# Kernel optimization log

Hardware: AMD Instinct MI355X
Metric: run time of the kernel (lower is better)

The kernel has to match this reference:

```python
import jax, jax.numpy as jnp
import numpy as np
from jax.scipy.stats import norm

B, IN, H0, H1, OUT = 1024, 2048, 4096, 4096, 1000
EPS_CDF = 1e-5
DECAY = 0.01
NEG_SLOPE = 0.01  # LeakyReLU default slope


def setup_inputs() -> dict:
    key = jax.random.key(0)
    ks = iter(jax.random.split(key, 40))
    rn = lambda shp, s=1.0: s * jax.random.normal(next(ks), shp, dtype=jnp.float32)
    inp = {}
    inp['x'] = rn((B, IN))
    inp['z_w'] = rn((IN,), 0.02)
    for nm, (o, i) in zip(['0', '1', 'o'], [(H0, IN), (H1, H0), (OUT, H1)]):
        inp['w_mu' + nm] = rn((o, i), 0.02)
        inp['w_ls' + nm] = rn((o, i), 0.1) - 2.0  # log-sigma ~ -2 => sigma ~ 0.13
        inp['b_mu' + nm] = rn((o,), 0.02)
        inp['b_ls' + nm] = rn((o,), 0.1) - 2.0
        inp['eps_w' + nm] = rn((o, i))
        inp['eps_b' + nm] = rn((o,))
    inp['pfz0'] = jax.random.uniform(next(ks), (B, H0), dtype=jnp.float32)
    inp['pfz1'] = jax.random.uniform(next(ks), (B, H1), dtype=jnp.float32)
    inp['y'] = jax.random.randint(next(ks), (B,), 0, OUT, dtype=jnp.int32)
    inp['mz0'] = jax.random.randint(next(ks), (B, H0), 0, 2, dtype=jnp.int32)
    inp['mz1'] = jax.random.randint(next(ks), (B, H1), 0, 2, dtype=jnp.int32)
    inp['mask_mu0'] = jax.random.randint(next(ks), (H0,), 0, 2, dtype=jnp.int32)
    inp['mask_mu1'] = jax.random.randint(next(ks), (H1,), 0, 2, dtype=jnp.int32)
    inp['data_set_size'] = 60000
    return inp


def _bayes_layer(h, w_mu, w_ls, b_mu, b_ls, eps_w, eps_b, mz, mask_mu, pfz):
    sw = jnp.exp(w_ls)
    sb = jnp.exp(b_ls)
    w = w_mu + sw * eps_w          # reparameterized weight sample
    b = b_mu + sb * eps_b
    h = h @ w.T + b                # F.linear
    h = jnp.where(h >= 0, h, NEG_SLOPE * h)  # LeakyReLU
    mzf = mz.astype(h.dtype)
    m = mzf * mask_mu.astype(h.dtype)[None, :]   # [B, h]
    mult = m.shape[1] / (m.sum(1) + 1e-6)        # rescale multiplier per sample
    h = h * m * mult[:, None]
    # GFN forward-flow log-prob of the z-mask
    p = jnp.clip(pfz, 1e-6, 1.0 - 1e-6)
    flow = (mzf * jnp.log(p) + (1.0 - mzf) * jnp.log(1.0 - p)).sum()
    # Gaussian CDF likelihood of sampled weights/biases (finite-difference density)
    pw = norm.cdf(w + EPS_CDF, w_mu, sw) - norm.cdf(w - EPS_CDF, w_mu, sw)
    pb = norm.cdf(b + EPS_CDF, b_mu, sb) - norm.cdf(b - EPS_CDF, b_mu, sb)
    flow = flow + jnp.log(pw).sum() + jnp.log(pb).sum()
    return h, flow


def reference(x, z_w, w_mu0, w_ls0, b_mu0, b_ls0, eps_w0, eps_b0,
              w_mu1, w_ls1, b_mu1, b_ls1, eps_w1, eps_b1,
              w_muo, w_lso, b_muo, b_lso, eps_wo, eps_bo,
              pfz0, pfz1, y, mz0, mz1, mask_mu0, mask_mu1, data_set_size):
    loss = (x @ z_w).sum()  # total flow estimator Z
    h, f0 = _bayes_layer(x, w_mu0, w_ls0, b_mu0, b_ls0, eps_w0, eps_b0, mz0, mask_mu0, pfz0)
    loss = loss + f0
    h, f1 = _bayes_layer(h, w_mu1, w_ls1, b_mu1, b_ls1, eps_w1, eps_b1, mz1, mask_mu1, pfz1)
    loss = loss + f1
    # output BayesLinear (sampled)
    wo = w_muo + jnp.exp(w_lso) * eps_wo
    bo = b_muo + jnp.exp(b_lso) * eps_bo
    pred = h @ wo.T + bo  # [B, OUT]
    logp = jax.nn.log_softmax(pred, axis=-1)
    ce = -jnp.take_along_axis(logp, y[:, None].astype(jnp.int32), axis=1).mean()
    loss = loss + jnp.float32(data_set_size) * ce  # NLL
    wd = DECAY * ((w_mu0 ** 2).sum() + jnp.exp(w_ls0).sum()
                  + (w_mu1 ** 2).sum() + jnp.exp(w_ls1).sum())
    loss = (loss + wd) ** 2
    return pred, loss
```

## Files before the change

kernel.cpp:

```cpp
#include <hip/hip_runtime.h>
#include <math.h>

#define B_SZ 1024
#define IN_SZ 2048
#define H0_SZ 4096
#define H1_SZ 4096
#define OUT_SZ 1000

typedef _Float16 f16;
typedef __attribute__((ext_vector_type(4))) _Float16 f16x4;
typedef __attribute__((ext_vector_type(8))) _Float16 f16x8;
typedef __attribute__((ext_vector_type(4))) float f32x4;

#define OFF_N0     0ULL
#define OFF_N1     4ULL
#define OFF_MSUM0  256ULL
#define OFF_MSUM1  4352ULL
#define OFF_CPOS0  8448ULL
#define OFF_CPOS1  24832ULL
#define OFF_IDX0   41216ULL
#define OFF_IDX1   57600ULL
#define OFF_PXZ    73984ULL
#define OFF_PFL    82176ULL
#define OFF_PCE    98560ULL
#define OFF_PB     106752ULL
#define OFF_PW     107776ULL
#define OFF_BS0    370688ULL
#define OFF_BS1    387072ULL
#define OFF_BSO    403456ULL
#define OFF_XH     407552ULL
#define OFF_XL     4601856ULL
#define OFF_H0H    8796160ULL
#define OFF_H0L    17184768ULL
#define OFF_H1H    25573376ULL
#define OFF_H1L    33961984ULL
#define OFF_W0CH   42350592ULL
#define OFF_W0CL   59127808ULL
#define OFF_W1CH   75905024ULL
#define OFF_W1CL   109459456ULL
#define OFF_WOCH   143013888ULL
#define OFF_WOCL   151402496ULL
#define OFF_PART   159791104ULL

#define PSTRIDE_H  2560
#define PSTRIDE_O  1024

#define PA_W0   1024
#define PA_FL0  1280
#define PA_SX   1536
#define PA_B0   1552
#define L0_G    640
#define L0_W1   1664
#define L0_FL1  1920
#define L0_B1   1936
#define L1_G    640
#define L1_WO   890
#define L1_BO   894

__device__ __forceinline__ void gload_lds16(const void* g, void* l)
{
    __builtin_amdgcn_global_load_lds((const __attribute__((address_space(1))) void*)g,
                                     (__attribute__((address_space(3))) void*)l, 16, 0, 0);
}

__device__ __forceinline__ void reduce4_store(double v0, double v1, double v2, double v3,
                                              double* dst)
{
    __shared__ double sh[4][4];
    double v[4] = {v0, v1, v2, v3};
    int lane = threadIdx.x & 63, wid = threadIdx.x >> 6;
#pragma unroll
    for (int a = 0; a < 4; ++a) {
        double x = v[a];
#pragma unroll
        for (int o = 32; o > 0; o >>= 1) x += __shfl_down(x, o, 64);
        if (lane == 0) sh[a][wid] = x;
    }
    __syncthreads();
    if (threadIdx.x == 0) {
        dst[0] = sh[0][0] + sh[0][1] + sh[0][2] + sh[0][3];
        dst[1] = sh[1][0] + sh[1][1] + sh[1][2] + sh[1][3];
        dst[2] = sh[2][0] + sh[2][1] + sh[2][2] + sh[2][3];
        dst[3] = sh[3][0] + sh[3][1] + sh[3][2] + sh[3][3];
    }
}

__device__ __forceinline__ void reduce1_store(double v, double* dst)
{
    __shared__ double sh1[4];
    int lane = threadIdx.x & 63, wid = threadIdx.x >> 6;
#pragma unroll
    for (int o = 32; o > 0; o >>= 1) v += __shfl_down(v, o, 64);
    if (lane == 0) sh1[wid] = v;
    __syncthreads();
    if (threadIdx.x == 0) dst[0] = sh1[0] + sh1[1] + sh1[2] + sh1[3];
}

__global__ __launch_bounds__(1024) void idxbuild_kernel(
    const int* __restrict__ mask0, const int* __restrict__ mask1,
    int* __restrict__ cpos0, int* __restrict__ idx0, int* __restrict__ n0,
    int* __restrict__ cpos1, int* __restrict__ idx1, int* __restrict__ n1)
{
    __shared__ int sh[1024];
    const int t = threadIdx.x;
    const int pass = blockIdx.x;
    const int* mask = pass ? mask1 : mask0;
    int* cpos = pass ? cpos1 : cpos0;
    int* idx = pass ? idx1 : idx0;
    int* np = pass ? n1 : n0;
    int4 m = ((const int4*)mask)[t];
    int s = m.x + m.y + m.z + m.w;
    sh[t] = s;
    __syncthreads();
    for (int o = 1; o < 1024; o <<= 1) {
        int v = (t >= o) ? sh[t - o] : 0;
        __syncthreads();
        sh[t] += v;
        __syncthreads();
    }
    int run = sh[t] - s;
    int4 cp;
    cp.x = run; cp.y = run + m.x; cp.z = cp.y + m.y; cp.w = cp.z + m.z;
    ((int4*)cpos)[t] = cp;
    if (m.x) idx[cp.x] = 4 * t + 0;
    if (m.y) idx[cp.y] = 4 * t + 1;
    if (m.z) idx[cp.z] = 4 * t + 2;
    if (m.w) idx[cp.w] = 4 * t + 3;
    if (t == 1023) *np = sh[1023];
}


__device__ void role_splitx(int rb, const float4* x, const float4* zw,
                            f16x4* xh, f16x4* xl, double* pxz)
{
    const int n4 = B_SZ * IN_SZ / 4;
    double s = 0;
    int i = rb * 256 + threadIdx.x;
    const int stride = 256 * 256;
    for (; i < n4; i += stride) {
        float4 v = x[i];
        float4 z = zw[i & (IN_SZ / 4 - 1)];
        s += (double)((v.x * z.x + v.y * z.y) + (v.z * z.z + v.w * z.w));
        f16 h0 = (f16)v.x, h1 = (f16)v.y, h2 = (f16)v.z, h3 = (f16)v.w;
        f16x4 hv = {h0, h1, h2, h3};
        f16x4 lv = {(f16)(v.x - (float)h0), (f16)(v.y - (float)h1),
                    (f16)(v.z - (float)h2), (f16)(v.w - (float)h3)};
        xh[i] = hv; xl[i] = lv;
    }
    reduce1_store(s, pxz + rb);
}

__device__ void role_flow4(int bb, const int* mz, const float* pfz, const int* maskmu,
                           float* msum, double* pfl)
{
    const int w = threadIdx.x >> 6, lane = threadIdx.x & 63;
    const int r = bb * 4 + w;
    const int4* m4 = (const int4*)(mz + (size_t)r * 4096);
    const float4* p4 = (const float4*)(pfz + (size_t)r * 4096);
    const int4* k4 = (const int4*)maskmu;
    int s = 0;
    double fl = 0;
    for (int i = lane; i < 1024; i += 64) {
        int4 m = m4[i];
        float4 p = p4[i];
        int4 k = k4[i];
        s += m.x * k.x + m.y * k.y + m.z * k.z + m.w * k.w;
        float a0 = fminf(fmaxf(p.x, 1e-6f), 1.0f - 1e-6f);
        float a1 = fminf(fmaxf(p.y, 1e-6f), 1.0f - 1e-6f);
        float a2 = fminf(fmaxf(p.z, 1e-6f), 1.0f - 1e-6f);
        float a3 = fminf(fmaxf(p.w, 1e-6f), 1.0f - 1e-6f);
        float g0 = logf(m.x ? a0 : 1.0f - a0);
        float g1 = logf(m.y ? a1 : 1.0f - a1);
        float g2 = logf(m.z ? a2 : 1.0f - a2);
        float g3 = logf(m.w ? a3 : 1.0f - a3);
        fl += (double)((g0 + g1) + (g2 + g3));
    }
#pragma unroll
    for (int o = 32; o > 0; o >>= 1) s += __shfl_down(s, o, 64);
    if (lane == 0) msum[r] = (float)s;
    reduce1_store(fl, pfl + bb);
}

template <int RED>
__device__ void role_bsample(int rb, const float* bmu, const float* bls, const float* beps,
                             float* out, int n, double* pb)
{
    int i = rb * 256 + threadIdx.x;
    float l = 0.f, e = 0.f;
    if (i < n) {
        l = bls[i]; e = beps[i];
        out[i] = fmaf(__expf(l), e, bmu[i]);
    }
    if (RED) {
        double sls = (i < n) ? (double)l : 0.0;
        double se2 = (i < n) ? (double)e * e : 0.0;
        reduce4_store(sls, se2, 0.0, 0.0, pb + (size_t)rb * 4);
    }
}

__device__ void role_w04(int bb, const float* mu, const float* ls, const float* eps,
                         const int* maskR, const int* cposR, f16* hi, double* pw)
{
    double sls = 0, se2 = 0, smu2 = 0, sex = 0;
#pragma unroll
    for (int rr = 0; rr < 4; ++rr) {
        const int r = bb * 4 + rr;
        const size_t rbb = (size_t)r * IN_SZ;
        const float4* m4 = (const float4*)(mu + rbb);
        const float4* l4 = (const float4*)(ls + rbb);
        const float4* e4 = (const float4*)(eps + rbb);
        const bool wr_ = maskR[r] != 0;
        const int drow = cposR[r];
        f16* hrow = hi + (size_t)drow * IN_SZ;
        for (int i = threadIdx.x; i < IN_SZ / 4; i += 256) {
            float4 m = m4[i], l = l4[i], e = e4[i];
            float g0 = __expf(l.x), g1 = __expf(l.y), g2 = __expf(l.z), g3 = __expf(l.w);
            float w0 = fmaf(g0, e.x, m.x), w1 = fmaf(g1, e.y, m.y);
            float w2 = fmaf(g2, e.z, m.z), w3 = fmaf(g3, e.w, m.w);
            sls += (double)((l.x + l.y) + (l.z + l.w));
            se2 += (double)((e.x * e.x + e.y * e.y) + (e.z * e.z + e.w * e.w));
            smu2 += (double)((m.x * m.x + m.y * m.y) + (m.z * m.z + m.w * m.w));
            sex += (double)((g0 + g1) + (g2 + g3));
            if (wr_) {
                f16x4 hv = {(f16)w0, (f16)w1, (f16)w2, (f16)w3};
                *(f16x4*)(hrow + i * 4) = hv;
            }
        }
    }
    reduce4_store(sls, se2, smu2, sex, pw + (size_t)bb * 4);
}

template <int ROWC, int RED>
__device__ void role_colc4(int bb, const float* mu, const float* ls, const float* eps,
                           const int* maskR, const int* cposR,
                           const int* maskC, const int* cposC, const int* pNc,
                           f16* hi, double* pw, f16* ldsH)
{
    const int t = threadIdx.x;
    const f16x8 z8 = {0, 0, 0, 0, 0, 0, 0, 0};
    for (int i = t; i < 512; i += 256) ((f16x8*)ldsH)[i] = z8;
    __syncthreads();
    double sls = 0, se2 = 0, smu2 = 0, sex = 0;
    const int n8 = ((*pNc + 127) >> 7) << 4;
#pragma unroll
    for (int rr = 0; rr < 4; ++rr) {
        const int r = bb * 4 + rr;
        const size_t rbb = (size_t)r * 4096;
        const float4* m4 = (const float4*)(mu + rbb);
        const float4* l4 = (const float4*)(ls + rbb);
        const float4* e4 = (const float4*)(eps + rbb);
        const bool wr_ = ROWC ? (maskR[r] != 0) : true;
        const int drow = ROWC ? cposR[r] : r;
        for (int i = t; i < 1024; i += 256) {
            float4 m = m4[i], l = l4[i], e = e4[i];
            float g0 = __expf(l.x), g1 = __expf(l.y), g2 = __expf(l.z), g3 = __expf(l.w);
            float w0 = fmaf(g0, e.x, m.x), w1 = fmaf(g1, e.y, m.y);
            float w2 = fmaf(g2, e.z, m.z), w3 = fmaf(g3, e.w, m.w);
            if (RED) {
                sls += (double)((l.x + l.y) + (l.z + l.w));
                se2 += (double)((e.x * e.x + e.y * e.y) + (e.z * e.z + e.w * e.w));
                smu2 += (double)((m.x * m.x + m.y * m.y) + (m.z * m.z + m.w * m.w));
                sex += (double)((g0 + g1) + (g2 + g3));
            }
            if (wr_) {
                int4 mc = ((const int4*)maskC)[i];
                int4 cp = ((const int4*)cposC)[i];
                if (mc.x) ldsH[cp.x] = (f16)w0;
                if (mc.y) ldsH[cp.y] = (f16)w1;
                if (mc.z) ldsH[cp.z] = (f16)w2;
                if (mc.w) ldsH[cp.w] = (f16)w3;
            }
        }
        __syncthreads();
        if (wr_) {
            f16x8* hd = (f16x8*)(hi + (size_t)drow * 4096);
            for (int i = t; i < n8; i += 256) hd[i] = ((const f16x8*)ldsH)[i];
        }
        __syncthreads();
    }
    if (RED) reduce4_store(sls, se2, smu2, sex, pw + (size_t)bb * 4);
}

template <int NSPLIT>
__device__ void gemm_body(int bid, f16* ldsbase,
                          const f16* Ah, const f16* Al, int SA,
                          const f16* Wh, int SW,
                          const int* pN, int NFIX, const int* pK, int KFIX,
                          float* P0, float* P1, float* P2, float* P3,
                          float* P4, float* P5, float* P6, float* P7, int pstride)
{
    const int c8 = bid & 7, j = bid >> 3;
    int nt, mt, z;
    if (NSPLIT == 4) {
        const int p = c8 + 8 * (j % 10);
        nt = p >> 2; z = p & 3; mt = j / 10;
    } else {
        const int p = c8 + 8 * (j & 7);
        nt = p >> 3; z = p & 7; mt = j >> 3;
    }
    const int nvalid = pN ? *pN : NFIX;
    const int bn = nt * 128;
    if (bn >= nvalid) return;
    const int bm = mt * 128;
    const int kvalid = pK ? *pK : KFIX;
    const int ktiles = (kvalid + 31) >> 5;
    const int prt = (ktiles + NSPLIT - 1) / NSPLIT;
    const int kt0 = z * prt;
    const int kt1 = min(ktiles, kt0 + prt);
    float* Cf = (z == 0) ? P0 : (z == 1) ? P1 : (z == 2) ? P2 : (z == 3) ? P3
              : (z == 4) ? P4 : (z == 5) ? P5 : (z == 6) ? P6 : P7;

    const int tid = threadIdx.x;
    const int wv = tid >> 6, lane = tid & 63;
    const int wr = wv >> 1, wc = wv & 1;
    const int l15 = lane & 15, l4 = lane >> 4;

    const f16* sg[6];
    int ldst[6];
#pragma unroll
    for (int i = 0; i < 6; ++i) {
        const int c = wv * 6 + i;
        const int plane = c >> 3, cidx = c & 7;
        const f16* base = (plane == 0) ? Ah : (plane == 1) ? Al : Wh;
        const int S_ = (plane < 2) ? SA : SW;
        const int rowb = (plane < 2) ? bm : bn;
        sg[i] = base + (size_t)(rowb + cidx * 16 + l15) * S_ + l4 * 8;
        ldst[i] = c * 512 + lane * 8;
    }

#define STAGE(KT, B) do { \
        _Pragma("unroll") \
        for (int i_ = 0; i_ < 6; ++i_) \
            gload_lds16(sg[i_] + (size_t)(KT) * 32, ldsbase + (B) * 12288 + ldst[i_]); \
    } while (0)

    f32x4 acc[4][4];
#pragma unroll
    for (int m = 0; m < 4; ++m)
#pragma unroll
        for (int n = 0; n < 4; ++n) acc[m][n] = (f32x4){0.f, 0.f, 0.f, 0.f};

    if (kt0 < kt1) {
        STAGE(kt0, 0);
        int cur = 0;
        for (int kt = kt0; kt < kt1; ++kt) {
            asm volatile("s_waitcnt vmcnt(0)" ::: "memory");
            __builtin_amdgcn_s_barrier();
            __builtin_amdgcn_sched_barrier(0);
            if (kt + 1 < kt1) STAGE(kt + 1, cur ^ 1);
            __builtin_amdgcn_sched_barrier(0);
            const f16* L = ldsbase + cur * 12288;
            f16x8 ah[4], al[4], wh[4];
#pragma unroll
            for (int m = 0; m < 4; ++m) {
                ah[m] = *(const f16x8*)(L + (wr * 4 + m) * 512 + lane * 8);
                al[m] = *(const f16x8*)(L + 4096 + (wr * 4 + m) * 512 + lane * 8);
            }
#pragma unroll
            for (int n = 0; n < 4; ++n)
                wh[n] = *(const f16x8*)(L + 8192 + (wc * 4 + n) * 512 + lane * 8);
            __builtin_amdgcn_s_setprio(1);
#pragma unroll
            for (int m = 0; m < 4; ++m)
#pragma unroll
                for (int n = 0; n < 4; ++n)
                    acc[m][n] = __builtin_amdgcn_mfma_f32_16x16x32_f16(ah[m], wh[n], acc[m][n], 0, 0, 0);
#pragma unroll
            for (int m = 0; m < 4; ++m)
#pragma unroll
                for (int n = 0; n < 4; ++n)
                    acc[m][n] = __builtin_amdgcn_mfma_f32_16x16x32_f16(al[m], wh[n], acc[m][n], 0, 0, 0);
            __builtin_amdgcn_s_setprio(0);
            cur ^= 1;
        }
    }
#undef STAGE

#pragma unroll
    for (int n = 0; n < 4; ++n) {
        const int c = bn + wc * 64 + n * 16 + l15;
        if (c >= pstride) continue;
#pragma unroll
        for (int m = 0; m < 4; ++m)
#pragma unroll
            for (int j2 = 0; j2 < 4; ++j2) {
                const int row = bm + wr * 64 + m * 16 + l4 * 4 + j2;
                Cf[(size_t)row * pstride + c] = acc[m][n][j2];
            }
    }
}

__global__ __launch_bounds__(256) void prepA_kernel(
    const float* __restrict__ x, const float* __restrict__ zw,
    const float* __restrict__ wmu0, const float* __restrict__ wls0, const float* __restrict__ weps0,
    const float* __restrict__ bmu0, const float* __restrict__ bls0, const float* __restrict__ beps0,
    const float* __restrict__ pfz0, const int* __restrict__ mz0,
    const int* __restrict__ mmu0, const int* __restrict__ cpos0,
    f16* __restrict__ xh, f16* __restrict__ xl, f16* __restrict__ w0ch,
    float* __restrict__ bs0, float* __restrict__ msum0,
    double* __restrict__ PXZ, double* __restrict__ PFL,
    double* __restrict__ PB, double* __restrict__ PW)
{
    const int b = blockIdx.x;
    if (b < PA_W0) {
        role_w04(b, wmu0, wls0, weps0, mmu0, cpos0, w0ch, PW);
    } else if (b < PA_FL0) {
        role_flow4(b - PA_W0, mz0, pfz0, mmu0, msum0, PFL);
    } else if (b < PA_SX) {
        role_splitx(b - PA_FL0, (const float4*)x, (const float4*)zw,
                    (f16x4*)xh, (f16x4*)xl, PXZ);
    } else {
        role_bsample<1>(b - PA_SX, bmu0, bls0, beps0, bs0, H0_SZ, PB);
    }
}

__global__ __launch_bounds__(256, 3) void gemmL0_kernel(
    const f16* __restrict__ xh, const f16* __restrict__ xl, const f16* __restrict__ w0ch,
    const int* __restrict__ n0p,
    float* __restrict__ A0, float* __restrict__ A1,
    float* __restrict__ A2, float* __restrict__ A3,
    const float* __restrict__ wmu1, const float* __restrict__ wls1, const float* __restrict__ weps1,
    const float* __restrict__ bmu1, const float* __restrict__ bls1, const float* __restrict__ beps1,
    const float* __restrict__ pfz1, const int* __restrict__ mz1,
    const int* __restrict__ mmu0, const int* __restrict__ mmu1,
    const int* __restrict__ cpos0, const int* __restrict__ cpos1,
    f16* __restrict__ w1ch, float* __restrict__ bs1, float* __restrict__ msum1,
    double* __restrict__ PFL, double* __restrict__ PB, double* __restrict__ PW)
{
    __shared__ __align__(16) f16 lds[2][12288];
    const int b = blockIdx.x;
    if (b < L0_G) {
        gemm_body<4>(b, &lds[0][0], xh, xl, IN_SZ, w0ch, IN_SZ, n0p, 0, nullptr, IN_SZ,
                     A0, A1, A2, A3, nullptr, nullptr, nullptr, nullptr, PSTRIDE_H);
    } else if (b < L0_W1) {
        role_colc4<1, 1>(b - L0_G, wmu1, wls1, weps1, mmu1, cpos1, mmu0, cpos0, n0p,
                         w1ch, PW + (size_t)4096 * 4, &lds[0][0]);
    } else if (b < L0_FL1) {
        role_flow4(b - L0_W1, mz1, pfz1, mmu1, msum1, PFL + 1024);
    } else {
        role_bsample<1>(b - L0_FL1, bmu1, bls1, beps1, bs1, H1_SZ, PB + 16 * 4);
    }
}

__global__ __launch_bounds__(256, 3) void gemmL1_kernel(
    const f16* __restrict__ h0h, const f16* __restrict__ h0l, const f16* __restrict__ w1ch,
    const int* __restrict__ n1p, const int* __restrict__ n0p,
    float* __restrict__ B0, float* __restrict__ B1,
    float* __restrict__ B2, float* __restrict__ B3,
    const float* __restrict__ wmuo, const float* __restrict__ wlso, const float* __restrict__ wepso,
    const float* __restrict__ bmuo, const float* __restrict__ blso, const float* __restrict__ bepso,
    const int* __restrict__ mmu1, const int* __restrict__ cpos1,
    f16* __restrict__ woch, float* __restrict__ bso)
{
    __shared__ __align__(16) f16 lds[2][12288];
    const int b = blockIdx.x;
    if (b < L1_G) {
        gemm_body<4>(b, &lds[0][0], h0h, h0l, 4096, w1ch, 4096, n1p, 0, n0p, 0,
                     B0, B1, B2, B3, nullptr, nullptr, nullptr, nullptr, PSTRIDE_H);
    } else if (b < L1_WO) {
        role_colc4<0, 0>(b - L1_G, wmuo, wlso, wepso, nullptr, nullptr, mmu1, cpos1, n1p,
                         woch, nullptr, &lds[0][0]);
    } else {
        role_bsample<0>(b - L1_WO, bmuo, blso, bepso, bso, OUT_SZ, nullptr);
    }
}

__global__ __launch_bounds__(256, 3) void gemmLo_kernel(
    const f16* __restrict__ h1h, const f16* __restrict__ h1l, const f16* __restrict__ woch,
    const int* __restrict__ n1p,
    float* __restrict__ Q0, float* __restrict__ Q1, float* __restrict__ Q2, float* __restrict__ Q3,
    float* __restrict__ Q4, float* __restrict__ Q5, float* __restrict__ Q6, float* __restrict__ Q7)
{
    __shared__ __align__(16) f16 lds[2][12288];
    gemm_body<8>(blockIdx.x, &lds[0][0], h1h, h1l, 4096, woch, 4096, nullptr, OUT_SZ, n1p, 0,
                 Q0, Q1, Q2, Q3, Q4, Q5, Q6, Q7, PSTRIDE_O);
}

__global__ __launch_bounds__(256) void combine4_kernel(
    const float* __restrict__ PA, const float* __restrict__ PB,
    const float* __restrict__ PC, const float* __restrict__ PD, int pstride,
    const float* __restrict__ bsamp, const int* __restrict__ idx,
    const int* __restrict__ mz, const float* __restrict__ msum,
    const int* __restrict__ pN,
    f16* __restrict__ Chh, f16* __restrict__ Chl)
{
    const int nv = *pN;
    const int bn = blockIdx.x * 64;
    const int bm = blockIdx.y * 64;
    const int t = threadIdx.x;
    const int c0 = bn + (t & 15) * 4;
    const int r0 = bm + (t >> 4);
#pragma unroll
    for (int rr = 0; rr < 4; ++rr) {
        const int row = r0 + rr * 16;
        const float mult = 4096.0f / (msum[row] + 1e-6f);
        float sv[4] = {0.f, 0.f, 0.f, 0.f};
        if (c0 < pstride) {
            float4 a = *(const float4*)(PA + (size_t)row * pstride + c0);
            float4 b = *(const float4*)(PB + (size_t)row * pstride + c0);
            float4 c = *(const float4*)(PC + (size_t)row * pstride + c0);
            float4 d = *(const float4*)(PD + (size_t)row * pstride + c0);
            sv[0] = (a.x + b.x) + (c.x + d.x);
            sv[1] = (a.y + b.y) + (c.y + d.y);
            sv[2] = (a.z + b.z) + (c.z + d.z);
            sv[3] = (a.w + b.w) + (c.w + d.w);
        }
        f16 hh[4], ll[4];
#pragma unroll
        for (int jj = 0; jj < 4; ++jj) {
            const int c = c0 + jj;
            float v = 0.f;
            if (c < nv) {
                const int orig = idx[c];
                v = sv[jj] + bsamp[orig];
                v = v >= 0.f ? v : 0.01f * v;
                v = v * (float)mz[(size_t)row * 4096 + orig] * mult;
            }
            hh[jj] = (f16)v;
            ll[jj] = (f16)(v - (float)hh[jj]);
        }
        f16x4 hv = {hh[0], hh[1], hh[2], hh[3]};
        f16x4 lv = {ll[0], ll[1], ll[2], ll[3]};
        *(f16x4*)(Chh + (size_t)row * 4096 + c0) = hv;
        *(f16x4*)(Chl + (size_t)row * 4096 + c0) = lv;
    }
}

__global__ __launch_bounds__(256) void ce_fused8_kernel(
    const float* __restrict__ Q0, const float* __restrict__ Q1,
    const float* __restrict__ Q2, const float* __restrict__ Q3,
    const float* __restrict__ Q4, const float* __restrict__ Q5,
    const float* __restrict__ Q6, const float* __restrict__ Q7,
    const float* __restrict__ bso, const int* __restrict__ y,
    float* __restrict__ pred, double* __restrict__ pce)
{
    const int b = blockIdx.x;
    float mx = -1e30f;
    for (int jj = threadIdx.x; jj < OUT_SZ; jj += 256) {
        const size_t o = (size_t)b * PSTRIDE_O + jj;
        float v = ((Q0[o] + Q1[o]) + (Q2[o] + Q3[o]))
                + ((Q4[o] + Q5[o]) + (Q6[o] + Q7[o])) + bso[jj];
        pred[(size_t)b * OUT_SZ + jj] = v;
        mx = fmaxf(mx, v);
    }
#pragma unroll
    for (int o = 32; o > 0; o >>= 1) mx = fmaxf(mx, __shfl_down(mx, o, 64));
    __shared__ float sm[4];
    if ((threadIdx.x & 63) == 0) sm[threadIdx.x >> 6] = mx;
    __syncthreads();
    mx = fmaxf(fmaxf(sm[0], sm[1]), fmaxf(sm[2], sm[3]));
    double se = 0;
    for (int jj = threadIdx.x; jj < OUT_SZ; jj += 256)
        se += (double)__expf(pred[(size_t)b * OUT_SZ + jj] - mx);
#pragma unroll
    for (int o = 32; o > 0; o >>= 1) se += __shfl_down(se, o, 64);
    __shared__ double sd[4];
    if ((threadIdx.x & 63) == 0) sd[threadIdx.x >> 6] = se;
    __syncthreads();
    if (threadIdx.x == 0) {
        double lse = (double)mx + log(sd[0] + sd[1] + sd[2] + sd[3]);
        pce[b] = lse - (double)pred[(size_t)b * OUT_SZ + y[b]];
    }
}

__global__ __launch_bounds__(256) void finalize_kernel(
    const double* __restrict__ PXZ, const double* __restrict__ PFL,
    const double* __restrict__ PCE, const double* __restrict__ PB,
    const double* __restrict__ PW, const int* __restrict__ dss, float* __restrict__ out)
{
    const int t = threadIdx.x;
    double xz = 0, fl = 0, ce = 0, ls = 0, e2 = 0, mu2 = 0, ex = 0;
    xz += PXZ[t];
    fl += PFL[t] + PFL[1024 + t];
    for (int i = t; i < 1024; i += 256) ce += PCE[i];
    for (int i = t; i < 1024; i += 256) {
        const double* p0 = PW + (size_t)i * 4;
        const double* p1 = PW + (size_t)(4096 + i) * 4;
        ls += p0[0] + p1[0];
        e2 += p0[1] + p1[1];
        mu2 += p0[2] + p1[2];
        ex += p0[3] + p1[3];
    }
    if (t < 32) { ls += PB[t * 4]; e2 += PB[t * 4 + 1]; }
    __shared__ double sh[7][4];
    double v[7] = {xz, fl, ce, ls, e2, mu2, ex};
    const int lane = t & 63, wid = t >> 6;
#pragma unroll
    for (int a = 0; a < 7; ++a) {
        double x = v[a];
#pragma unroll
        for (int o = 32; o > 0; o >>= 1) x += __shfl_down(x, o, 64);
        if (lane == 0) sh[a][wid] = x;
    }
    __syncthreads();
    if (t == 0) {
        double T[7];
#pragma unroll
        for (int a = 0; a < 7; ++a) T[a] = sh[a][0] + sh[a][1] + sh[a][2] + sh[a][3];
        const double NTOT = 25174016.0;
        double cst = NTOT * (log(2.0e-5) - 0.91893853320467274178);
        double loss = T[0]
                    + cst - T[3] - 0.5 * T[4]
                    + T[1]
                    + (double)(*dss) * (T[2] / (double)B_SZ)
                    + 0.01 * (T[5] + T[6]);
        out[(size_t)B_SZ * OUT_SZ] = (float)(loss * loss);
    }
}

extern "C" void kernel_launch(void* const* d_in, const int* in_sizes, int n_in,
                              void* d_out, int out_size, void* d_ws, size_t ws_size,
                              hipStream_t stream)
{
    const float* x = (const float*)d_in[0];
    const float* zw = (const float*)d_in[1];
    const float* wmu0 = (const float*)d_in[2];
    const float* wls0 = (const float*)d_in[3];
    const float* bmu0 = (const float*)d_in[4];
    const float* bls0 = (const float*)d_in[5];
    const float* weps0 = (const float*)d_in[6];
    const float* beps0 = (const float*)d_in[7];
    const float* wmu1 = (const float*)d_in[8];
    const float* wls1 = (const float*)d_in[9];
    const float* bmu1 = (const float*)d_in[10];
    const float* bls1 = (const float*)d_in[11];
    const float* weps1 = (const float*)d_in[12];
    const float* beps1 = (const float*)d_in[13];
    const float* wmuo = (const float*)d_in[14];
    const float* wlso = (const float*)d_in[15];
    const float* bmuo = (const float*)d_in[16];
    const float* blso = (const float*)d_in[17];
    const float* wepso = (const float*)d_in[18];
    const float* bepso = (const float*)d_in[19];
    const float* pfz0 = (const float*)d_in[20];
    const float* pfz1 = (const float*)d_in[21];
    const int* y = (const int*)d_in[22];
    const int* mz0 = (const int*)d_in[23];
    const int* mz1 = (const int*)d_in[24];
    const int* mmu0 = (const int*)d_in[25];
    const int* mmu1 = (const int*)d_in[26];
    const int* dss = (const int*)d_in[27];

    char* ws = (char*)d_ws;
    int* n0p = (int*)(ws + OFF_N0);
    int* n1p = (int*)(ws + OFF_N1);
    float* msum0 = (float*)(ws + OFF_MSUM0);
    float* msum1 = (float*)(ws + OFF_MSUM1);
    int* cpos0 = (int*)(ws + OFF_CPOS0);
    int* cpos1 = (int*)(ws + OFF_CPOS1);
    int* idx0 = (int*)(ws + OFF_IDX0);
    int* idx1 = (int*)(ws + OFF_IDX1);
    double* PXZ = (double*)(ws + OFF_PXZ);
    double* PFL = (double*)(ws + OFF_PFL);
    double* PCE = (double*)(ws + OFF_PCE);
    double* PB = (double*)(ws + OFF_PB);
    double* PW = (double*)(ws + OFF_PW);
    float* bs0 = (float*)(ws + OFF_BS0);
    float* bs1 = (float*)(ws + OFF_BS1);
    float* bso = (float*)(ws + OFF_BSO);
    f16* xh = (f16*)(ws + OFF_XH);
    f16* xl = (f16*)(ws + OFF_XL);
    f16* h0h = (f16*)(ws + OFF_H0H);
    f16* h0l = (f16*)(ws + OFF_H0L);
    f16* h1h = (f16*)(ws + OFF_H1H);
    f16* h1l = (f16*)(ws + OFF_H1L);
    f16* w0ch = (f16*)(ws + OFF_W0CH);
    f16* w1ch = (f16*)(ws + OFF_W1CH);
    f16* woch = (f16*)(ws + OFF_WOCH);
    float* out = (float*)d_out;

    float* A0 = (float*)(ws + OFF_H1H);
    float* A1 = (float*)(ws + OFF_PART);
    float* A2 = (float*)(ws + OFF_W0CL);
    float* A3 = (float*)(ws + OFF_W1CL);
    float* B0 = (float*)(ws + OFF_W0CH);
    float* B1 = (float*)(ws + OFF_W0CL);
    float* B2 = (float*)(ws + OFF_W1CL);
    float* B3 = (float*)(ws + OFF_PART);
    float* Q[8];
    for (int i = 0; i < 8; ++i) Q[i] = (float*)(ws + OFF_W0CH + (size_t)i * 4194304ULL);

    idxbuild_kernel<<<2, 1024, 0, stream>>>(mmu0, mmu1, cpos0, idx0, n0p, cpos1, idx1, n1p);

    prepA_kernel<<<PA_B0, 256, 0, stream>>>(
        x, zw, wmu0, wls0, weps0, bmu0, bls0, beps0,
        pfz0, mz0, mmu0, cpos0,
        xh, xl, w0ch, bs0, msum0, PXZ, PFL, PB, PW);

    gemmL0_kernel<<<L0_B1, 256, 0, stream>>>(
        xh, xl, w0ch, n0p, A0, A1, A2, A3,
        wmu1, wls1, weps1, bmu1, bls1, beps1,
        pfz1, mz1, mmu0, mmu1, cpos0, cpos1,
        w1ch, bs1, msum1, PFL, PB, PW);
    combine4_kernel<<<dim3(40, 16), 256, 0, stream>>>(
        A0, A1, A2, A3, PSTRIDE_H, bs0, idx0, mz0, msum0, n0p, h0h, h0l);

    gemmL1_kernel<<<L1_BO, 256, 0, stream>>>(
        h0h, h0l, w1ch, n1p, n0p, B0, B1, B2, B3,
        wmuo, wlso, wepso, bmuo, blso, bepso,
        mmu1, cpos1, woch, bso);
    combine4_kernel<<<dim3(40, 16), 256, 0, stream>>>(
        B0, B1, B2, B3, PSTRIDE_H, bs1, idx1, mz1, msum1, n1p, h1h, h1l);

    gemmLo_kernel<<<512, 256, 0, stream>>>(
        h1h, h1l, woch, n1p, Q[0], Q[1], Q[2], Q[3], Q[4], Q[5], Q[6], Q[7]);

    ce_fused8_kernel<<<B_SZ, 256, 0, stream>>>(Q[0], Q[1], Q[2], Q[3], Q[4], Q[5], Q[6], Q[7],
                                               bso, y, out, PCE);
    finalize_kernel<<<1, 256, 0, stream>>>(PXZ, PFL, PCE, PB, PW, dss, out);
}
```

Measured before the change: 252.7 us.

## Merge mask index build into pre-pass kernel and move side roles out of GEMMs

The separate 1024-thread idxbuild kernel becomes a 256-thread role inside a new pre0 kernel. That kernel also runs the x split, both flow reductions and all three bias samples. W0 preparation moves into its own kernel, and the flow/bias roles are removed from the layer GEMM kernels, so those launches carry only GEMM and weight-convert blocks. The aim is to cut the idxbuild launch and shorten the GEMM-phase kernels. The cost is an extra prepW0 launch, and the W0 conversion no longer overlaps with the x split.

```diff
diff --git a/kernel.cpp b/kernel.cpp
--- a/kernel.cpp
+++ b/kernel.cpp
@@ -45,17 +45,17 @@
 #define PSTRIDE_H  2560
 #define PSTRIDE_O  1024
 
-#define PA_W0   1024
-#define PA_FL0  1280
-#define PA_SX   1536
-#define PA_B0   1552
+#define P0_IDX  2
+#define P0_SX   258
+#define P0_FL0  514
+#define P0_FL1  770
+#define P0_B0   786
+#define P0_B1   802
+#define P0_BO   806
 #define L0_G    640
 #define L0_W1   1664
-#define L0_FL1  1920
-#define L0_B1   1936
 #define L1_G    640
 #define L1_WO   890
-#define L1_BO   894
 
 __device__ __forceinline__ void gload_lds16(const void* g, void* l)
 {
@@ -96,37 +96,47 @@
     if (threadIdx.x == 0) dst[0] = sh1[0] + sh1[1] + sh1[2] + sh1[3];
 }
 
-__global__ __launch_bounds__(1024) void idxbuild_kernel(
-    const int* __restrict__ mask0, const int* __restrict__ mask1,
-    int* __restrict__ cpos0, int* __restrict__ idx0, int* __restrict__ n0,
-    int* __restrict__ cpos1, int* __restrict__ idx1, int* __restrict__ n1)
-{
-    __shared__ int sh[1024];
+__device__ void role_idx256(int pass,
+                            const int* __restrict__ mask0, const int* __restrict__ mask1,
+                            int* __restrict__ cpos0, int* __restrict__ idx0, int* __restrict__ n0,
+                            int* __restrict__ cpos1, int* __restrict__ idx1, int* __restrict__ n1)
+{
+    __shared__ int sh[256];
     const int t = threadIdx.x;
-    const int pass = blockIdx.x;
     const int* mask = pass ? mask1 : mask0;
     int* cpos = pass ? cpos1 : cpos0;
     int* idx = pass ? idx1 : idx0;
     int* np = pass ? n1 : n0;
-    int4 m = ((const int4*)mask)[t];
-    int s = m.x + m.y + m.z + m.w;
+    const int4* m4 = (const int4*)mask;
+    int4 q[4];
+#pragma unroll
+    for (int jj = 0; jj < 4; ++jj) q[jj] = m4[t * 4 + jj];
+    int s = 0;
+#pragma unroll
+    for (int jj = 0; jj < 4; ++jj) s += q[jj].x + q[jj].y + q[jj].z + q[jj].w;
     sh[t] = s;
     __syncthreads();
-    for (int o = 1; o < 1024; o <<= 1) {
+    for (int o = 1; o < 256; o <<= 1) {
         int v = (t >= o) ? sh[t - o] : 0;
         __syncthreads();
         sh[t] += v;
         __syncthreads();
     }
     int run = sh[t] - s;
-    int4 cp;
-    cp.x = run; cp.y = run + m.x; cp.z = cp.y + m.y; cp.w = cp.z + m.z;
-    ((int4*)cpos)[t] = cp;
-    if (m.x) idx[cp.x] = 4 * t + 0;
-    if (m.y) idx[cp.y] = 4 * t + 1;
-    if (m.z) idx[cp.z] = 4 * t + 2;
-    if (m.w) idx[cp.w] = 4 * t + 3;
-    if (t == 1023) *np = sh[1023];
+#pragma unroll
+    for (int jj = 0; jj < 4; ++jj) {
+        int4 m = q[jj];
+        int4 cp;
+        cp.x = run; cp.y = run + m.x; cp.z = cp.y + m.y; cp.w = cp.z + m.z;
+        ((int4*)cpos)[t * 4 + jj] = cp;
+        const int e = 16 * t + 4 * jj;
+        if (m.x) idx[cp.x] = e + 0;
+        if (m.y) idx[cp.y] = e + 1;
+        if (m.z) idx[cp.z] = e + 2;
+        if (m.w) idx[cp.w] = e + 3;
+        run = cp.w + m.w;
+    }
+    if (t == 255) *np = sh[255];
 }
 
 
@@ -390,28 +400,46 @@
     }
 }
 
-__global__ __launch_bounds__(256) void prepA_kernel(
+__global__ __launch_bounds__(256) void pre0_kernel(
     const float* __restrict__ x, const float* __restrict__ zw,
+    const float* __restrict__ bmu0, const float* __restrict__ bls0, const float* __restrict__ beps0,
+    const float* __restrict__ bmu1, const float* __restrict__ bls1, const float* __restrict__ beps1,
+    const float* __restrict__ bmuo, const float* __restrict__ blso, const float* __restrict__ bepso,
+    const float* __restrict__ pfz0, const float* __restrict__ pfz1,
+    const int* __restrict__ mz0, const int* __restrict__ mz1,
+    const int* __restrict__ mmu0, const int* __restrict__ mmu1,
+    int* __restrict__ cpos0, int* __restrict__ idx0, int* __restrict__ n0p,
+    int* __restrict__ cpos1, int* __restrict__ idx1, int* __restrict__ n1p,
+    f16* __restrict__ xh, f16* __restrict__ xl,
+    float* __restrict__ bs0, float* __restrict__ bs1, float* __restrict__ bso,
+    float* __restrict__ msum0, float* __restrict__ msum1,
+    double* __restrict__ PXZ, double* __restrict__ PFL, double* __restrict__ PB)
+{
+    const int b = blockIdx.x;
+    if (b < P0_IDX) {
+        role_idx256(b, mmu0, mmu1, cpos0, idx0, n0p, cpos1, idx1, n1p);
+    } else if (b < P0_SX) {
+        role_splitx(b - P0_IDX, (const float4*)x, (const float4*)zw,
+                    (f16x4*)xh, (f16x4*)xl, PXZ);
+    } else if (b < P0_FL0) {
+        role_flow4(b - P0_SX, mz0, pfz0, mmu0, msum0, PFL);
+    } else if (b < P0_FL1) {
+        role_flow4(b - P0_FL0, mz1, pfz1, mmu1, msum1, PFL + 1024);
+    } else if (b < P0_B0) {
+        role_bsample<1>(b - P0_FL1, bmu0, bls0, beps0, bs0, H0_SZ, PB);
+    } else if (b < P0_B1) {
+        role_bsample<1>(b - P0_B0, bmu1, bls1, beps1, bs1, H1_SZ, PB + 16 * 4);
+    } else {
+        role_bsample<0>(b - P0_B1, bmuo, blso, bepso, bso, OUT_SZ, nullptr);
+    }
+}
+
+__global__ __launch_bounds__(256) void prepW0_kernel(
     const float* __restrict__ wmu0, const float* __restrict__ wls0, const float* __restrict__ weps0,
-    const float* __restrict__ bmu0, const float* __restrict__ bls0, const float* __restrict__ beps0,
-    const float* __restrict__ pfz0, const int* __restrict__ mz0,
     const int* __restrict__ mmu0, const int* __restrict__ cpos0,
-    f16* __restrict__ xh, f16* __restrict__ xl, f16* __restrict__ w0ch,
-    float* __restrict__ bs0, float* __restrict__ msum0,
-    double* __restrict__ PXZ, double* __restrict__ PFL,
-    double* __restrict__ PB, double* __restrict__ PW)
-{
-    const int b = blockIdx.x;
-    if (b < PA_W0) {
-        role_w04(b, wmu0, wls0, weps0, mmu0, cpos0, w0ch, PW);
-    } else if (b < PA_FL0) {
-        role_flow4(b - PA_W0, mz0, pfz0, mmu0, msum0, PFL);
-    } else if (b < PA_SX) {
-        role_splitx(b - PA_FL0, (const float4*)x, (const float4*)zw,
-                    (f16x4*)xh, (f16x4*)xl, PXZ);
-    } else {
-        role_bsample<1>(b - PA_SX, bmu0, bls0, beps0, bs0, H0_SZ, PB);
-    }
+    f16* __restrict__ w0ch, double* __restrict__ PW)
+{
+    role_w04(blockIdx.x, wmu0, wls0, weps0, mmu0, cpos0, w0ch, PW);
 }
 
 __global__ __launch_bounds__(256, 3) void gemmL0_kernel(
@@ -420,25 +448,18 @@
     float* __restrict__ A0, float* __restrict__ A1,
     float* __restrict__ A2, float* __restrict__ A3,
     const float* __restrict__ wmu1, const float* __restrict__ wls1, const float* __restrict__ weps1,
-    const float* __restrict__ bmu1, const float* __restrict__ bls1, const float* __restrict__ beps1,
-    const float* __restrict__ pfz1, const int* __restrict__ mz1,
     const int* __restrict__ mmu0, const int* __restrict__ mmu1,
     const int* __restrict__ cpos0, const int* __restrict__ cpos1,
-    f16* __restrict__ w1ch, float* __restrict__ bs1, float* __restrict__ msum1,
-    double* __restrict__ PFL, double* __restrict__ PB, double* __restrict__ PW)
+    f16* __restrict__ w1ch, double* __restrict__ PW)
 {
     __shared__ __align__(16) f16 lds[2][12288];
     const int b = blockIdx.x;
     if (b < L0_G) {
         gemm_body<4>(b, &lds[0][0], xh, xl, IN_SZ, w0ch, IN_SZ, n0p, 0, nullptr, IN_SZ,
                      A0, A1, A2, A3, nullptr, nullptr, nullptr, nullptr, PSTRIDE_H);
-    } else if (b < L0_W1) {
+    } else {
         role_colc4<1, 1>(b - L0_G, wmu1, wls1, weps1, mmu1, cpos1, mmu0, cpos0, n0p,
                          w1ch, PW + (size_t)4096 * 4, &lds[0][0]);
-    } else if (b < L0_FL1) {
-        role_flow4(b - L0_W1, mz1, pfz1, mmu1, msum1, PFL + 1024);
-    } else {
-        role_bsample<1>(b - L0_FL1, bmu1, bls1, beps1, bs1, H1_SZ, PB + 16 * 4);
     }
 }
 
@@ -448,20 +469,17 @@
     float* __restrict__ B0, float* __restrict__ B1,
     float* __restrict__ B2, float* __restrict__ B3,
     const float* __restrict__ wmuo, const float* __restrict__ wlso, const float* __restrict__ wepso,
-    const float* __restrict__ bmuo, const float* __restrict__ blso, const float* __restrict__ bepso,
     const int* __restrict__ mmu1, const int* __restrict__ cpos1,
-    f16* __restrict__ woch, float* __restrict__ bso)
+    f16* __restrict__ woch)
 {
     __shared__ __align__(16) f16 lds[2][12288];
     const int b = blockIdx.x;
     if (b < L1_G) {
         gemm_body<4>(b, &lds[0][0], h0h, h0l, 4096, w1ch, 4096, n1p, 0, n0p, 0,
                      B0, B1, B2, B3, nullptr, nullptr, nullptr, nullptr, PSTRIDE_H);
-    } else if (b < L1_WO) {
+    } else {
         role_colc4<0, 0>(b - L1_G, wmuo, wlso, wepso, nullptr, nullptr, mmu1, cpos1, n1p,
                          woch, nullptr, &lds[0][0]);
-    } else {
-        role_bsample<0>(b - L1_WO, bmuo, blso, bepso, bso, OUT_SZ, nullptr);
     }
 }
 
@@ -680,25 +698,25 @@
     float* Q[8];
     for (int i = 0; i < 8; ++i) Q[i] = (float*)(ws + OFF_W0CH + (size_t)i * 4194304ULL);
 
-    idxbuild_kernel<<<2, 1024, 0, stream>>>(mmu0, mmu1, cpos0, idx0, n0p, cpos1, idx1, n1p);
-
-    prepA_kernel<<<PA_B0, 256, 0, stream>>>(
-        x, zw, wmu0, wls0, weps0, bmu0, bls0, beps0,
-        pfz0, mz0, mmu0, cpos0,
-        xh, xl, w0ch, bs0, msum0, PXZ, PFL, PB, PW);
-
-    gemmL0_kernel<<<L0_B1, 256, 0, stream>>>(
+    pre0_kernel<<<P0_BO, 256, 0, stream>>>(
+        x, zw, bmu0, bls0, beps0, bmu1, bls1, beps1, bmuo, blso, bepso,
+        pfz0, pfz1, mz0, mz1, mmu0, mmu1,
+        cpos0, idx0, n0p, cpos1, idx1, n1p,
+        xh, xl, bs0, bs1, bso, msum0, msum1, PXZ, PFL, PB);
+
+    prepW0_kernel<<<1024, 256, 0, stream>>>(
+        wmu0, wls0, weps0, mmu0, cpos0, w0ch, PW);
+
+    gemmL0_kernel<<<L0_W1, 256, 0, stream>>>(
         xh, xl, w0ch, n0p, A0, A1, A2, A3,
-        wmu1, wls1, weps1, bmu1, bls1, beps1,
-        pfz1, mz1, mmu0, mmu1, cpos0, cpos1,
-        w1ch, bs1, msum1, PFL, PB, PW);
+        wmu1, wls1, weps1, mmu0, mmu1, cpos0, cpos1,
+        w1ch, PW);
     combine4_kernel<<<dim3(40, 16), 256, 0, stream>>>(
         A0, A1, A2, A3, PSTRIDE_H, bs0, idx0, mz0, msum0, n0p, h0h, h0l);
 
-    gemmL1_kernel<<<L1_BO, 256, 0, stream>>>(
+    gemmL1_kernel<<<L1_WO, 256, 0, stream>>>(
         h0h, h0l, w1ch, n1p, n0p, B0, B1, B2, B3,
-        wmuo, wlso, wepso, bmuo, blso, bepso,
-        mmu1, cpos1, woch, bso);
+        wmuo, wlso, wepso, mmu1, cpos1, woch);
     combine4_kernel<<<dim3(40, 16), 256, 0, stream>>>(
         B0, B1, B2, B3, PSTRIDE_H, bs1, idx1, mz1, msum1, n1p, h1h, h1l);
 
```

Measured after the change: 256.2 us. No clear change (+1.4%).
